# Optimization experiments

Hardware: AMD Instinct MI355X
Metric: run time of the kernel (lower is better)

The kernel has to match this reference:

```python
import jax, jax.numpy as jnp
import numpy as np

HIDDEN = 1024
NUM_HEADS = 16
HEAD_DIM = HIDDEN // NUM_HEADS  # 64
B, S = 4, 1024


def setup_inputs() -> dict:
    key = jax.random.key(0)
    ks = jax.random.split(key, 8)
    xavier = jax.nn.initializers.xavier_uniform()
    inputs = jax.random.normal(ks[0], (B, S, HIDDEN), dtype=jnp.float32)
    context = jax.random.normal(ks[1], (B, S, HIDDEN), dtype=jnp.float32)
    # multiplicative mask: 1 = attend, 0 = ignore (causal), broadcast over batch/heads
    mask = jnp.tril(jnp.ones((S, S), dtype=jnp.float32))[None, None, :, :]
    Wq = xavier(ks[2], (HIDDEN, HIDDEN), jnp.float32)
    bq = jnp.zeros((HIDDEN,), jnp.float32)
    Wk = xavier(ks[3], (HIDDEN, HEAD_DIM), jnp.float32)
    bk = jnp.zeros((HEAD_DIM,), jnp.float32)
    Wv = xavier(ks[4], (HIDDEN, HEAD_DIM), jnp.float32)
    bv = jnp.zeros((HEAD_DIM,), jnp.float32)
    Wo = xavier(ks[5], (HIDDEN, HIDDEN), jnp.float32)
    bo = jnp.zeros((HIDDEN,), jnp.float32)
    return {"inputs": inputs, "context": context, "mask": mask,
            "Wq": Wq, "bq": bq, "Wk": Wk, "bk": bk,
            "Wv": Wv, "bv": bv, "Wo": Wo, "bo": bo}


def reference(inputs, context, mask, Wq, bq, Wk, bk, Wv, bv, Wo, bo):
    query = inputs @ Wq + bq                      # (B, S, D)
    key = context @ Wk + bk                       # (B, S, D/H)
    value = context @ Wv + bv                     # (B, S, D/H)
    # MQA: broadcast single KV head to all query heads via interleaved repeat
    key = jnp.repeat(key, NUM_HEADS, axis=-1)     # (B, S, D)
    value = jnp.repeat(value, NUM_HEADS, axis=-1) # (B, S, D)
    bsz = query.shape[0]
    Lq, Lk = query.shape[1], key.shape[1]
    # faithful to original: plain reshape (not transpose) into heads
    qh = jnp.reshape(query, (bsz, NUM_HEADS, Lq, HEAD_DIM))
    kh = jnp.reshape(key, (bsz, NUM_HEADS, Lk, HEAD_DIM))
    vh = jnp.reshape(value, (bsz, NUM_HEADS, Lk, HEAD_DIM))
    # note: original scales by sqrt(key.shape[-1]) == sqrt(hidden_dim)
    scores = jnp.einsum('bhqd,bhkd->bhqk', qh, kh) / jnp.sqrt(jnp.float32(HIDDEN))
    scores = scores * mask                        # multiplicative mask
    attn = jax.nn.softmax(scores, axis=-1)        # (B, H, Lq, Lk)
    ctx = jnp.einsum('bhqk,bhkd->bhqd', attn, vh)
    ctx = jnp.reshape(ctx, (bsz, Lq, HIDDEN))
    outputs = ctx @ Wo + bo                       # (B, S, D)
    return outputs, attn
```

## Files before the change

kernel.cpp:

```cpp
#include <hip/hip_runtime.h>
#include <hip/hip_bf16.h>
#include <cstdint>

#define NHEADS 16
#define SEQ    1024
#define BATCH  4

__device__ __forceinline__ float wave_max(float v){
  #pragma unroll
  for (int off = 32; off > 0; off >>= 1) v = fmaxf(v, __shfl_xor(v, off));
  return v;
}
__device__ __forceinline__ float wave_sum(float v){
  #pragma unroll
  for (int off = 32; off > 0; off >>= 1) v += __shfl_xor(v, off);
  return v;
}

__global__ __launch_bounds__(256) void prep_kernel(
    const float* __restrict__ Wq, const float* __restrict__ bq,
    const float* __restrict__ Wo,
    float* __restrict__ WqSum, float* __restrict__ bqSum, float* __restrict__ WoSum)
{
  const int blk = blockIdx.x, tid = threadIdx.x;
  if (blk < 256){
    const int c = blk * 4 + (tid >> 6), g = tid & 63;
    const float* p = &Wq[(size_t)c * 1024 + (g << 4)];
    float s = 0.f;
    #pragma unroll
    for (int f = 0; f < 16; ++f) s += p[f];
    WqSum[c * 64 + g] = s;
  } else if (blk < 320){
    const int g = blk - 256;
    for (int m = tid; m < 1024; m += 256){
      float s = 0.f;
      #pragma unroll
      for (int f = 0; f < 16; ++f) s += Wo[(size_t)((g << 4) + f) * 1024 + m];
      WoSum[g * 1024 + m] = s;
    }
  } else {
    if (tid < 64){
      float s = 0.f;
      #pragma unroll
      for (int f = 0; f < 16; ++f) s += bq[(tid << 4) + f];
      bqSum[tid] = s;
    }
  }
}

__global__ __launch_bounds__(256) void qkv_split(
    const float* __restrict__ inputs, const float* __restrict__ context,
    const float* __restrict__ WqSum,
    const float* __restrict__ Wk, const float* __restrict__ Wv,
    float* __restrict__ part)
{
  __shared__ float As[16][64];
  __shared__ float Bs[16][64];
  const int z = blockIdx.y, sz = blockIdx.z;
  const float* A = (z == 0) ? inputs : context;
  const float* B = (z == 0) ? WqSum : ((z == 1) ? Wk : Wv);
  const int m0 = blockIdx.x * 64;
  const int ks = sz << 8;
  const int tid = threadIdx.x;
  const int tx = tid & 15, ty = tid >> 4;
  const int arow = tid >> 2, acg = (tid & 3) << 2;
  const int brow = tid >> 4, bcg = (tid & 15) << 2;

  float acc[4][4] = {};
  for (int t = 0; t < 16; ++t){
    const int k0 = ks + (t << 4);
    const float4 av  = *(const float4*)&A[(size_t)(m0 + arow) * 1024 + k0 + acg];
    const float4 bvv = *(const float4*)&B[(size_t)(k0 + brow) * 64 + bcg];
    As[acg + 0][arow] = av.x; As[acg + 1][arow] = av.y;
    As[acg + 2][arow] = av.z; As[acg + 3][arow] = av.w;
    *(float4*)&Bs[brow][bcg] = bvv;
    __syncthreads();
    #pragma unroll
    for (int kk = 0; kk < 16; ++kk){
      const float4 a  = *(const float4*)&As[kk][ty << 2];
      const float4 bb = *(const float4*)&Bs[kk][tx << 2];
      const float a_[4] = {a.x, a.y, a.z, a.w};
      const float b_[4] = {bb.x, bb.y, bb.z, bb.w};
      #pragma unroll
      for (int i = 0; i < 4; ++i)
        #pragma unroll
        for (int j = 0; j < 4; ++j) acc[i][j] += a_[i] * b_[j];
    }
    __syncthreads();
  }
  float* P = part + ((size_t)(z * 4 + sz) * 4096 + m0) * 64;
  #pragma unroll
  for (int i = 0; i < 4; ++i)
    *(float4*)&P[(size_t)((ty << 2) + i) * 64 + (tx << 2)] =
      make_float4(acc[i][0], acc[i][1], acc[i][2], acc[i][3]);
}

__global__ __launch_bounds__(256) void qkv_reduce(
    const float* __restrict__ part,
    const float* __restrict__ bqSum, const float* __restrict__ bk,
    const float* __restrict__ bv,
    float* __restrict__ Qs, float* __restrict__ Kv, float* __restrict__ Vv)
{
  const int z = blockIdx.y;
  const float* bias = (z == 0) ? bqSum : ((z == 1) ? bk : bv);
  float* O          = (z == 0) ? Qs    : ((z == 1) ? Kv : Vv);
  const int tid = threadIdx.x;
  const int row = blockIdx.x * 16 + (tid >> 4);
  const int c4  = (tid & 15) << 2;
  const size_t off = (size_t)row * 64 + c4;
  const size_t zb  = (size_t)z * 4 * 4096 * 64;
  float4 s = *(const float4*)&part[zb + off];
  #pragma unroll
  for (int p = 1; p < 4; ++p){
    const float4 t = *(const float4*)&part[zb + (size_t)p * 4096 * 64 + off];
    s.x += t.x; s.y += t.y; s.z += t.z; s.w += t.w;
  }
  const float4 bv4 = *(const float4*)&bias[c4];
  s.x += bv4.x; s.y += bv4.y; s.z += bv4.z; s.w += bv4.w;
  *(float4*)&O[off] = s;
}

__global__ __launch_bounds__(256) void attn_kernel(
    const float* __restrict__ Qs, const float* __restrict__ Kv,
    const float* __restrict__ Vv, float* __restrict__ Ctx,
    float* __restrict__ attnp)
{
  __shared__ float BmT[4][1024];
  __shared__ float VmT[4][1024];
  __shared__ float Aq[64][4];
  __shared__ float bsum[4][4];
  __shared__ float SufT[4][5];

  const int tid = threadIdx.x;
  const int qb = blockIdx.x;
  const int h  = blockIdx.y;
  const int b  = blockIdx.z;
  const int base = b * SEQ + h * 64;

  for (int idx = tid; idx < 4096; idx += 256){
    const int r = idx >> 6, c = idx & 63;
    const int k = (r << 4) + (c >> 2), e = c & 3;
    BmT[e][k] = Kv[(size_t)(base + r) * 64 + c];
    VmT[e][k] = Vv[(size_t)(base + r) * 64 + c];
  }
  {
    const int p_l = tid >> 6, g = tid & 63;
    Aq[(p_l << 4) + (g >> 2)][g & 3] = Qs[(size_t)(base + qb * 4 + p_l) * 64 + g];
  }
  __syncthreads();
  if (tid < 16){
    const int e = tid >> 2, jj = tid & 3;
    float s = 0.f;
    for (int kk = 0; kk < 256; ++kk) s += VmT[e][(jj << 8) + kk];
    bsum[e][jj] = s;
  }
  __syncthreads();
  if (tid < 4){
    float s = 0.f;
    SufT[tid][4] = 0.f;
    for (int jj = 3; jj >= 0; --jj){ s += bsum[tid][jj]; SufT[tid][jj] = s; }
  }
  __syncthreads();

  const int wave = tid >> 6, lane = tid & 63;
  for (int i = 0; i < 16; ++i){
    const int ql = (wave << 4) + i;
    const int q  = (qb << 6) + ql;
    const float4 a = *(const float4*)&Aq[ql][0];
    const int jdot = (q >> 8) + 1;
    float4 sv[4];
    float mloc = (q == 1023) ? -3.0e38f : 0.0f;
    #pragma unroll
    for (int j = 0; j < 4; ++j){
      if (j < jdot){
        const int k0 = (lane << 2) + (j << 8);
        const float4 b0 = *(const float4*)&BmT[0][k0];
        const float4 b1 = *(const float4*)&BmT[1][k0];
        const float4 b2 = *(const float4*)&BmT[2][k0];
        const float4 b3 = *(const float4*)&BmT[3][k0];
        float4 t;
        t.x = (a.x*b0.x + a.y*b1.x + a.z*b2.x + a.w*b3.x) * 0.03125f;
        t.y = (a.x*b0.y + a.y*b1.y + a.z*b2.y + a.w*b3.y) * 0.03125f;
        t.z = (a.x*b0.z + a.y*b1.z + a.z*b2.z + a.w*b3.z) * 0.03125f;
        t.w = (a.x*b0.w + a.y*b1.w + a.z*b2.w + a.w*b3.w) * 0.03125f;
        t.x = (k0     <= q) ? t.x : 0.0f;
        t.y = (k0 + 1 <= q) ? t.y : 0.0f;
        t.z = (k0 + 2 <= q) ? t.z : 0.0f;
        t.w = (k0 + 3 <= q) ? t.w : 0.0f;
        sv[j] = t;
        mloc = fmaxf(mloc, fmaxf(fmaxf(t.x, t.y), fmaxf(t.z, t.w)));
      }
    }
    const float m  = wave_max(mloc);
    const float em = __expf(-m);
    float Zl = 0.f, c0 = 0.f, c1 = 0.f, c2 = 0.f, c3 = 0.f;
    #pragma unroll
    for (int j = 0; j < 4; ++j){
      if (j < jdot){
        const int k0 = (lane << 2) + (j << 8);
        const float e0 = __expf(sv[j].x - m);
        const float e1 = __expf(sv[j].y - m);
        const float e2 = __expf(sv[j].z - m);
        const float e3 = __expf(sv[j].w - m);
        Zl += (e0 + e1) + (e2 + e3);
        const float4 v0 = *(const float4*)&VmT[0][k0];
        const float4 v1 = *(const float4*)&VmT[1][k0];
        const float4 v2 = *(const float4*)&VmT[2][k0];
        const float4 v3 = *(const float4*)&VmT[3][k0];
        c0 += e0*v0.x + e1*v0.y + e2*v0.z + e3*v0.w;
        c1 += e0*v1.x + e1*v1.y + e2*v1.z + e3*v1.w;
        c2 += e0*v2.x + e1*v2.y + e2*v2.z + e3*v2.w;
        c3 += e0*v3.x + e1*v3.y + e2*v3.z + e3*v3.w;
        sv[j] = make_float4(e0, e1, e2, e3);
      }
    }
    const int ktail = jdot << 8;
    const float Z = wave_sum(Zl) + em * (float)(1024 - ktail);
    c0 = wave_sum(c0) + em * SufT[0][jdot];
    c1 = wave_sum(c1) + em * SufT[1][jdot];
    c2 = wave_sum(c2) + em * SufT[2][jdot];
    c3 = wave_sum(c3) + em * SufT[3][jdot];
    const float invZ = 1.0f / Z;

    float* rowp = attnp + (((size_t)(b * NHEADS + h) << 10) + (size_t)q) * 1024;
    #pragma unroll
    for (int j = 0; j < 4; ++j){
      if (j < jdot){
        const int k0 = (lane << 2) + (j << 8);
        *(float4*)(rowp + k0) = make_float4(sv[j].x * invZ, sv[j].y * invZ,
                                            sv[j].z * invZ, sv[j].w * invZ);
      }
    }
    const float fv = em * invZ;
    const float4 fillv = make_float4(fv, fv, fv, fv);
    for (int rr = 0; rr < 4 - jdot; ++rr){
      *(float4*)(rowp + ktail + (rr << 8) + (lane << 2)) = fillv;
    }
    if (lane == 0){
      *(float4*)&Ctx[(size_t)(base + (q >> 4)) * 64 + ((q & 15) << 2)] =
        make_float4(c0 * invZ, c1 * invZ, c2 * invZ, c3 * invZ);
    }
  }
}

__global__ __launch_bounds__(256) void out_gemm(
    const float* __restrict__ Ctx, const float* __restrict__ WoSum,
    const float* __restrict__ bo, float* __restrict__ outp)
{
  __shared__ float Cs[64][68];
  __shared__ float Ws[64][128];
  const int tid = threadIdx.x;
  const int m0 = blockIdx.x * 64, n0 = blockIdx.y * 128;

  for (int t = tid; t < 1024; t += 256){
    const int row = t >> 4, c4 = (t & 15) << 2;
    const float4 v = *(const float4*)&Ctx[(size_t)(m0 + row) * 64 + c4];
    Cs[c4 + 0][row] = v.x; Cs[c4 + 1][row] = v.y;
    Cs[c4 + 2][row] = v.z; Cs[c4 + 3][row] = v.w;
  }
  for (int t = tid; t < 2048; t += 256){
    const int row = t >> 5, c4 = (t & 31) << 2;
    *(float4*)&Ws[row][c4] = *(const float4*)&WoSum[(size_t)row * 1024 + n0 + c4];
  }
  __syncthreads();

  const int tx = tid & 31, ty = tid >> 5;
  float acc[8][4] = {};
  for (int kk = 0; kk < 64; ++kk){
    const float4 bb = *(const float4*)&Ws[kk][tx << 2];
    const float4 a0 = *(const float4*)&Cs[kk][ty << 3];
    const float4 a1 = *(const float4*)&Cs[kk][(ty << 3) + 4];
    const float a_[8] = {a0.x, a0.y, a0.z, a0.w, a1.x, a1.y, a1.z, a1.w};
    const float b_[4] = {bb.x, bb.y, bb.z, bb.w};
    #pragma unroll
    for (int i = 0; i < 8; ++i)
      #pragma unroll
      for (int j = 0; j < 4; ++j) acc[i][j] += a_[i] * b_[j];
  }
  const float4 bov = *(const float4*)&bo[n0 + (tx << 2)];
  #pragma unroll
  for (int i = 0; i < 8; ++i){
    float4 r;
    r.x = acc[i][0] + bov.x; r.y = acc[i][1] + bov.y;
    r.z = acc[i][2] + bov.z; r.w = acc[i][3] + bov.w;
    *(float4*)&outp[(size_t)(m0 + (ty << 3) + i) * 1024 + n0 + (tx << 2)] = r;
  }
}

extern "C" void kernel_launch(void* const* d_in, const int* in_sizes, int n_in,
                              void* d_out, int out_size, void* d_ws, size_t ws_size,
                              hipStream_t stream)
{
  const float* inputs  = (const float*)d_in[0];
  const float* context = (const float*)d_in[1];
  const float* Wq = (const float*)d_in[3];
  const float* bq = (const float*)d_in[4];
  const float* Wk = (const float*)d_in[5];
  const float* bk = (const float*)d_in[6];
  const float* Wv = (const float*)d_in[7];
  const float* bv = (const float*)d_in[8];
  const float* Wo = (const float*)d_in[9];
  const float* bo = (const float*)d_in[10];

  float* outp  = (float*)d_out;
  float* attnp = outp + (size_t)BATCH * SEQ * 1024;

  float* ws    = (float*)d_ws;
  float* WqSum = ws;
  float* bqSum = ws + 65536;
  float* WoSum = ws + 65600;
  float* Qs    = ws + 131136;
  float* Kv    = ws + 393280;
  float* Vv    = ws + 655424;
  float* Ctx   = ws + 917568;
  float* part  = ws + 1179712;

  prep_kernel<<<dim3(321), dim3(256), 0, stream>>>(Wq, bq, Wo, WqSum, bqSum, WoSum);
  qkv_split <<<dim3(64, 3, 4), dim3(256), 0, stream>>>(inputs, context, WqSum,
                                                       Wk, Wv, part);
  qkv_reduce<<<dim3(256, 3), dim3(256), 0, stream>>>(part, bqSum, bk, bv,
                                                     Qs, Kv, Vv);
  attn_kernel<<<dim3(16, 16, 4), dim3(256), 0, stream>>>(Qs, Kv, Vv, Ctx, attnp);
  out_gemm  <<<dim3(64, 8), dim3(256), 0, stream>>>(Ctx, WoSum, bo, outp);
}
```

Before: 133.0 us.

## Fuse split-K reduction into attention kernel and double-buffer QKV GEMM tiles

```diff
diff --git a/kernel.cpp b/kernel.cpp
--- a/kernel.cpp
+++ b/kernel.cpp
@@ -54,8 +54,8 @@
     const float* __restrict__ Wk, const float* __restrict__ Wv,
     float* __restrict__ part)
 {
-  __shared__ float As[16][64];
-  __shared__ float Bs[16][64];
+  __shared__ float As[2][16][68];
+  __shared__ float Bs[2][16][68];
   const int z = blockIdx.y, sz = blockIdx.z;
   const float* A = (z == 0) ? inputs : context;
   const float* B = (z == 0) ? WqSum : ((z == 1) ? Wk : Wv);
@@ -66,19 +66,25 @@
   const int arow = tid >> 2, acg = (tid & 3) << 2;
   const int brow = tid >> 4, bcg = (tid & 15) << 2;
 
+  float4 av  = *(const float4*)&A[(size_t)(m0 + arow) * 1024 + ks + acg];
+  float4 bvv = *(const float4*)&B[(size_t)(ks + brow) * 64 + bcg];
+  As[0][acg + 0][arow] = av.x; As[0][acg + 1][arow] = av.y;
+  As[0][acg + 2][arow] = av.z; As[0][acg + 3][arow] = av.w;
+  *(float4*)&Bs[0][brow][bcg] = bvv;
+  __syncthreads();
+
   float acc[4][4] = {};
   for (int t = 0; t < 16; ++t){
-    const int k0 = ks + (t << 4);
-    const float4 av  = *(const float4*)&A[(size_t)(m0 + arow) * 1024 + k0 + acg];
-    const float4 bvv = *(const float4*)&B[(size_t)(k0 + brow) * 64 + bcg];
-    As[acg + 0][arow] = av.x; As[acg + 1][arow] = av.y;
-    As[acg + 2][arow] = av.z; As[acg + 3][arow] = av.w;
-    *(float4*)&Bs[brow][bcg] = bvv;
-    __syncthreads();
+    const int cur = t & 1;
+    if (t < 15){
+      const int k0 = ks + ((t + 1) << 4);
+      av  = *(const float4*)&A[(size_t)(m0 + arow) * 1024 + k0 + acg];
+      bvv = *(const float4*)&B[(size_t)(k0 + brow) * 64 + bcg];
+    }
     #pragma unroll
     for (int kk = 0; kk < 16; ++kk){
-      const float4 a  = *(const float4*)&As[kk][ty << 2];
-      const float4 bb = *(const float4*)&Bs[kk][tx << 2];
+      const float4 a  = *(const float4*)&As[cur][kk][ty << 2];
+      const float4 bb = *(const float4*)&Bs[cur][kk][tx << 2];
       const float a_[4] = {a.x, a.y, a.z, a.w};
       const float b_[4] = {bb.x, bb.y, bb.z, bb.w};
       #pragma unroll
@@ -86,6 +92,11 @@
         #pragma unroll
         for (int j = 0; j < 4; ++j) acc[i][j] += a_[i] * b_[j];
     }
+    if (t < 15){
+      As[cur ^ 1][acg + 0][arow] = av.x; As[cur ^ 1][acg + 1][arow] = av.y;
+      As[cur ^ 1][acg + 2][arow] = av.z; As[cur ^ 1][acg + 3][arow] = av.w;
+      *(float4*)&Bs[cur ^ 1][brow][bcg] = bvv;
+    }
     __syncthreads();
   }
   float* P = part + ((size_t)(z * 4 + sz) * 4096 + m0) * 64;
@@ -95,38 +106,14 @@
       make_float4(acc[i][0], acc[i][1], acc[i][2], acc[i][3]);
 }
 
-__global__ __launch_bounds__(256) void qkv_reduce(
+__global__ __launch_bounds__(256) void attn_kernel(
     const float* __restrict__ part,
     const float* __restrict__ bqSum, const float* __restrict__ bk,
     const float* __restrict__ bv,
-    float* __restrict__ Qs, float* __restrict__ Kv, float* __restrict__ Vv)
-{
-  const int z = blockIdx.y;
-  const float* bias = (z == 0) ? bqSum : ((z == 1) ? bk : bv);
-  float* O          = (z == 0) ? Qs    : ((z == 1) ? Kv : Vv);
-  const int tid = threadIdx.x;
-  const int row = blockIdx.x * 16 + (tid >> 4);
-  const int c4  = (tid & 15) << 2;
-  const size_t off = (size_t)row * 64 + c4;
-  const size_t zb  = (size_t)z * 4 * 4096 * 64;
-  float4 s = *(const float4*)&part[zb + off];
-  #pragma unroll
-  for (int p = 1; p < 4; ++p){
-    const float4 t = *(const float4*)&part[zb + (size_t)p * 4096 * 64 + off];
-    s.x += t.x; s.y += t.y; s.z += t.z; s.w += t.w;
-  }
-  const float4 bv4 = *(const float4*)&bias[c4];
-  s.x += bv4.x; s.y += bv4.y; s.z += bv4.z; s.w += bv4.w;
-  *(float4*)&O[off] = s;
-}
-
-__global__ __launch_bounds__(256) void attn_kernel(
-    const float* __restrict__ Qs, const float* __restrict__ Kv,
-    const float* __restrict__ Vv, float* __restrict__ Ctx,
-    float* __restrict__ attnp)
-{
-  __shared__ float BmT[4][1024];
-  __shared__ float VmT[4][1024];
+    float* __restrict__ Ctx, float* __restrict__ attnp)
+{
+  __shared__ float BmT[4][1032];
+  __shared__ float VmT[4][1032];
   __shared__ float Aq[64][4];
   __shared__ float bsum[4][4];
   __shared__ float SufT[4][5];
@@ -139,13 +126,24 @@
 
   for (int idx = tid; idx < 4096; idx += 256){
     const int r = idx >> 6, c = idx & 63;
+    const size_t off = (size_t)(base + r) * 64 + c;
+    float kacc = bk[c], vacc = bv[c];
+    #pragma unroll
+    for (int s = 0; s < 4; ++s){
+      kacc += part[(size_t)(4 + s) * 262144 + off];
+      vacc += part[(size_t)(8 + s) * 262144 + off];
+    }
     const int k = (r << 4) + (c >> 2), e = c & 3;
-    BmT[e][k] = Kv[(size_t)(base + r) * 64 + c];
-    VmT[e][k] = Vv[(size_t)(base + r) * 64 + c];
+    BmT[e][k] = kacc;
+    VmT[e][k] = vacc;
   }
   {
     const int p_l = tid >> 6, g = tid & 63;
-    Aq[(p_l << 4) + (g >> 2)][g & 3] = Qs[(size_t)(base + qb * 4 + p_l) * 64 + g];
+    float qacc = bqSum[g];
+    const size_t off = (size_t)(base + (qb << 2) + p_l) * 64 + g;
+    #pragma unroll
+    for (int s = 0; s < 4; ++s) qacc += part[(size_t)s * 262144 + off];
+    Aq[(p_l << 4) + (g >> 2)][g & 3] = qacc;
   }
   __syncthreads();
   if (tid < 16){
@@ -309,17 +307,13 @@
   float* WqSum = ws;
   float* bqSum = ws + 65536;
   float* WoSum = ws + 65600;
-  float* Qs    = ws + 131136;
-  float* Kv    = ws + 393280;
-  float* Vv    = ws + 655424;
-  float* Ctx   = ws + 917568;
-  float* part  = ws + 1179712;
+  float* Ctx   = ws + 131136;
+  float* part  = ws + 393280;
 
   prep_kernel<<<dim3(321), dim3(256), 0, stream>>>(Wq, bq, Wo, WqSum, bqSum, WoSum);
   qkv_split <<<dim3(64, 3, 4), dim3(256), 0, stream>>>(inputs, context, WqSum,
                                                        Wk, Wv, part);
-  qkv_reduce<<<dim3(256, 3), dim3(256), 0, stream>>>(part, bqSum, bk, bv,
-                                                     Qs, Kv, Vv);
-  attn_kernel<<<dim3(16, 16, 4), dim3(256), 0, stream>>>(Qs, Kv, Vv, Ctx, attnp);
+  attn_kernel<<<dim3(16, 16, 4), dim3(256), 0, stream>>>(part, bqSum, bk, bv,
+                                                         Ctx, attnp);
   out_gemm  <<<dim3(64, 8), dim3(256), 0, stream>>>(Ctx, WoSum, bo, outp);
 }
```

After: 135.4 us. Within noise of the previous version (+1.8%).
